# Kernel optimization log

Hardware: AMD Instinct MI355X
Metric: run time of the kernel (lower is better)

## Reference

```python
import jax, jax.numpy as jnp
import numpy as np

B, T, D, H, W = 256, 512, 64, 128, 256

def _init_linear(key, out_dim, in_dim):
    lim = 1.0 / np.sqrt(in_dim)
    return jax.random.uniform(key, (out_dim, in_dim), jnp.float32, -lim, lim)

def setup_inputs():
    key = jax.random.key(0)
    ks = jax.random.split(key, 12)
    inp = {}
    inp['ts'] = jnp.arange(T, dtype=jnp.float32)
    for n, k in zip(['coeffs_d', 'coeffs_c', 'coeffs_b', 'coeffs_a'], ks[:4]):
        inp[n] = jax.random.normal(k, (B, T - 1, D), jnp.float32) * 0.05
    # initial MLP: D -> W -> W -> H (relu hidden, identity final)
    inp['i_w0'] = _init_linear(ks[4], W, D); inp['i_b0'] = jnp.zeros((W,), jnp.float32)
    inp['i_w1'] = _init_linear(ks[5], W, W); inp['i_b1'] = jnp.zeros((W,), jnp.float32)
    inp['i_w2'] = _init_linear(ks[6], H, W); inp['i_b2'] = jnp.zeros((H,), jnp.float32)
    # func MLP: H -> W -> W -> H*D (softplus hidden, tanh final)
    inp['f_w0'] = _init_linear(ks[7], W, H); inp['f_b0'] = jnp.zeros((W,), jnp.float32)
    inp['f_w1'] = _init_linear(ks[8], W, W); inp['f_b1'] = jnp.zeros((W,), jnp.float32)
    inp['f_w2'] = _init_linear(ks[9], H * D, W); inp['f_b2'] = jnp.zeros((H * D,), jnp.float32)
    # readout linear: H -> 1
    inp['l_w'] = _init_linear(ks[10], 1, H); inp['l_b'] = jnp.zeros((1,), jnp.float32)
    return inp

def reference(ts, coeffs_d, coeffs_c, coeffs_b, coeffs_a,
              i_w0, i_b0, i_w1, i_b1, i_w2, i_b2,
              f_w0, f_b0, f_w1, f_b1, f_w2, f_b2,
              l_w, l_b):
    dt = ts[1] - ts[0]
    # cubic spline value at t=ts[0]: interval 0, frac 0 -> a[0]
    x0 = coeffs_a[:, 0, :]  # [B, D]
    h = jax.nn.relu(x0 @ i_w0.T + i_b0)
    h = jax.nn.relu(h @ i_w1.T + i_b1)
    y0 = h @ i_w2.T + i_b2  # [B, H]

    def step(carry, _):
        t, y = carry
        # cubic spline derivative at t: b + 2c*frac + 3d*frac^2 on interval idx
        idx = jnp.clip(jnp.searchsorted(ts, t, side='right') - 1, 0, T - 2)
        frac = t - ts[idx]
        deriv = coeffs_b[:, idx] + 2.0 * coeffs_c[:, idx] * frac + 3.0 * coeffs_d[:, idx] * (frac * frac)  # [B, D]
        # vector field f(y): [B, H, D]
        g = jax.nn.softplus(y @ f_w0.T + f_b0)
        g = jax.nn.softplus(g @ f_w1.T + f_b1)
        f = jnp.tanh(g @ f_w2.T + f_b2).reshape(B, H, D)
        # Euler step: y1 = y + (f @ dX/dt) * dt
        y1 = y + jnp.einsum('bhd,bd->bh', f, deriv) * dt
        return (t + dt, y1), y1

    _, ys = jax.lax.scan(step, (ts[0], y0), None, length=T)
    # prediction = sigmoid(linear(ys[-1]))[0], per batch element
    return jax.nn.sigmoid(ys[-1] @ l_w.T + l_b)[:, 0]  # [B]
```

## Files before the change

### kernel.cpp

```cpp
#include <hip/hip_runtime.h>
#include <hip/hip_bf16.h>
#include <stdint.h>


#define BB 256
#define DD 64
#define HH 128
#define WW 256
#define HD 8192
#define TSTEPS 512
#define PAD_Y 152
#define PAD_G 280
#define PAD_DV 68

typedef __bf16 bf16x8 __attribute__((ext_vector_type(8)));
typedef __bf16 bf16x4 __attribute__((ext_vector_type(4)));
typedef float f32x4 __attribute__((ext_vector_type(4)));

__device__ __forceinline__ float softplus_f(float x) {
  return (x > 15.f) ? x : __logf(1.f + __expf(x));
}
__device__ __forceinline__ float tanh_f(float x) {
  float e = __expf(2.f * x);
  return 1.f - 2.f / (e + 1.f);
}
__device__ __forceinline__ float aloadf(const float* p) {
  return __hip_atomic_load(p, __ATOMIC_RELAXED, __HIP_MEMORY_SCOPE_AGENT);
}
__device__ __forceinline__ void astoref(float* p, float v) {
  __hip_atomic_store(p, v, __ATOMIC_RELAXED, __HIP_MEMORY_SCOPE_AGENT);
}
__device__ __forceinline__ uint32_t aloadu(const uint32_t* p) {
  return __hip_atomic_load(p, __ATOMIC_RELAXED, __HIP_MEMORY_SCOPE_AGENT);
}
__device__ __forceinline__ void astoreu(uint32_t* p, uint32_t v) {
  __hip_atomic_store(p, v, __ATOMIC_RELAXED, __HIP_MEMORY_SCOPE_AGENT);
}

__global__ void prep_kernel(const float* __restrict__ w0, const float* __restrict__ w1,
                            const float* __restrict__ w2,
                            __bf16* __restrict__ w0b, __bf16* __restrict__ w1b,
                            __bf16* __restrict__ w2b) {
  int stride = gridDim.x * blockDim.x;
  int i0 = blockIdx.x * blockDim.x + threadIdx.x;
  for (int i = i0; i < WW * HH; i += stride) w0b[i] = (__bf16)w0[i];
  for (int i = i0; i < WW * WW; i += stride) w1b[i] = (__bf16)w1[i];
  for (int i = i0; i < HD * WW; i += stride) w2b[i] = (__bf16)w2[i];
}

__global__ __launch_bounds__(256) void init_kernel(
    const float* __restrict__ ca, const float* __restrict__ iw0, const float* __restrict__ ib0,
    const float* __restrict__ iw1, const float* __restrict__ ib1,
    const float* __restrict__ iw2, const float* __restrict__ ib2,
    float* __restrict__ y0) {
  __shared__ float x0[DD];
  __shared__ float h0[WW];
  __shared__ float h1[WW];
  int b = blockIdx.x, t = threadIdx.x;
  if (t < DD) x0[t] = ca[((size_t)b * 511) * DD + t];
  __syncthreads();
  float a = ib0[t];
  for (int d = 0; d < DD; ++d) a = fmaf(x0[d], iw0[t * DD + d], a);
  h0[t] = fmaxf(a, 0.f);
  __syncthreads();
  a = ib1[t];
  for (int d = 0; d < WW; ++d) a = fmaf(h0[d], iw1[t * WW + d], a);
  h1[t] = fmaxf(a, 0.f);
  __syncthreads();
  if (t < HH) {
    a = ib2[t];
    for (int d = 0; d < WW; ++d) a = fmaf(h1[d], iw2[t * WW + d], a);
    y0[b * HH + t] = a;
  }
}

__global__ __launch_bounds__(512, 2) void step_persist(
    const __bf16* __restrict__ w0b, const __bf16* __restrict__ w1b, const __bf16* __restrict__ w2b,
    const float* __restrict__ fb0, const float* __restrict__ fb1, const float* __restrict__ fb2,
    const float* __restrict__ cbp, const float* __restrict__ ccp, const float* __restrict__ cdp,
    float* __restrict__ yA, float* __restrict__ pk, uint32_t* __restrict__ yflag)
{
  __shared__ __align__(16) __bf16 yb[32 * PAD_Y];
  __shared__ __align__(16) __bf16 g0s[32 * PAD_G];
  __shared__ __align__(16) __bf16 g1s[32 * PAD_G];
  __shared__ __align__(16) float dv[32 * PAD_DV];
  __shared__ float pbuf[8 * 32];

  const int tid = threadIdx.x;
  const int wv = tid >> 6;
  const int l = tid & 63;
  const int l16 = l & 15;
  const int lq = l >> 4;

  const int wid = blockIdx.x;
  const int grp = wid >> 5;
  const int j = wid & 31;
  const int rb = grp * 32;
  const int c0 = j * 256;

  bf16x8 w0f[4][2], w1f[8][2], w2f[8][2];
  #pragma unroll
  for (int c = 0; c < 2; ++c) {
    int col = wv * 32 + c * 16 + l16;
    #pragma unroll
    for (int kb = 0; kb < 4; ++kb)
      w0f[kb][c] = *(const bf16x8*)&w0b[col * HH + kb * 32 + lq * 8];
    #pragma unroll
    for (int kb = 0; kb < 8; ++kb)
      w1f[kb][c] = *(const bf16x8*)&w1b[col * WW + kb * 32 + lq * 8];
    #pragma unroll
    for (int kb = 0; kb < 8; ++kb)
      w2f[kb][c] = *(const bf16x8*)&w2b[(size_t)(c0 + col) * WW + kb * 32 + lq * 8];
  }
  f32x4 b0r[2], b1r[2], b2r[2];
  #pragma unroll
  for (int c = 0; c < 2; ++c) {
    b0r[c] = *(const f32x4*)&fb0[wv * 32 + c * 16 + lq * 4];
    b1r[c] = *(const f32x4*)&fb1[wv * 32 + c * 16 + lq * 4];
    b2r[c] = *(const f32x4*)&fb2[c0 + wv * 32 + c * 16 + lq * 4];
  }

  float yreg = 0.f;
  int myidx = 0;
  if (tid < 128) {
    int r = tid & 31, hl = tid >> 5;
    myidx = (rb + r) * HH + (4 * j + hl);
    yreg = yA[myidx];
    astoref(&pk[myidx], yreg);
  }
  __syncthreads();
  if (tid == 0) astoreu(&yflag[grp * 32 + j], 1u);

  const int ps = tid & 31;
  const int pw = tid >> 5;
  const uint32_t* myflag = &yflag[grp * 32 + ps];

  for (int k = 0; k < TSTEPS; ++k) {
    const uint32_t want = (uint32_t)(k + 1);
    const float* src = pk + (size_t)(k & 1) * (BB * HH);
    float* dst = pk + (size_t)((k + 1) & 1) * (BB * HH);

    float dreg[4];
    {
      int kk = (k <= 510) ? k : 510;
      #pragma unroll
      for (int q = 0; q < 4; ++q) {
        int i = tid + q * 512;
        int r = i >> 6, d = i & (DD - 1);
        int off = ((rb + r) * 511 + kk) * DD + d;
        float v = cbp[off];
        if (k == 511) v += 2.f * ccp[off] + 3.f * cdp[off];
        dreg[q] = v;
      }
    }

    {
      int spins = 0;
      while (aloadu(myflag) < want) {
        __builtin_amdgcn_s_sleep(1);
        if (++spins > (1 << 20)) break;
      }
      __asm__ __volatile__("" ::: "memory");
      #pragma unroll
      for (int r2 = 0; r2 < 2; ++r2) {
        int row = 2 * pw + r2;
        const float* ysrc = &src[(rb + row) * HH + 4 * ps];
        bf16x4 o;
        #pragma unroll
        for (int q = 0; q < 4; ++q) o[q] = (__bf16)aloadf(&ysrc[q]);
        *(bf16x4*)&yb[row * PAD_Y + 4 * ps] = o;
      }
    }
    __syncthreads();

    {
      f32x4 acc[2][2] = {};
      #pragma unroll
      for (int kb = 0; kb < 4; ++kb) {
        bf16x8 y0 = *(const bf16x8*)&yb[l16 * PAD_Y + kb * 32 + lq * 8];
        bf16x8 y1 = *(const bf16x8*)&yb[(16 + l16) * PAD_Y + kb * 32 + lq * 8];
        #pragma unroll
        for (int c = 0; c < 2; ++c) {
          acc[c][0] = __builtin_amdgcn_mfma_f32_16x16x32_bf16(w0f[kb][c], y0, acc[c][0], 0, 0, 0);
          acc[c][1] = __builtin_amdgcn_mfma_f32_16x16x32_bf16(w0f[kb][c], y1, acc[c][1], 0, 0, 0);
        }
      }
      #pragma unroll
      for (int c = 0; c < 2; ++c)
        #pragma unroll
        for (int bt = 0; bt < 2; ++bt) {
          bf16x4 o;
          #pragma unroll
          for (int r = 0; r < 4; ++r)
            o[r] = (__bf16)softplus_f(acc[c][bt][r] + b0r[c][r]);
          *(bf16x4*)&g0s[(bt * 16 + l16) * PAD_G + wv * 32 + c * 16 + lq * 4] = o;
        }
    }
    #pragma unroll
    for (int q = 0; q < 4; ++q) {
      int i = tid + q * 512;
      dv[(i >> 6) * PAD_DV + (i & (DD - 1))] = dreg[q];
    }
    __syncthreads();

    {
      f32x4 acc[2][2] = {};
      #pragma unroll
      for (int kb = 0; kb < 8; ++kb) {
        bf16x8 a0 = *(const bf16x8*)&g0s[l16 * PAD_G + kb * 32 + lq * 8];
        bf16x8 a1 = *(const bf16x8*)&g0s[(16 + l16) * PAD_G + kb * 32 + lq * 8];
        #pragma unroll
        for (int c = 0; c < 2; ++c) {
          acc[c][0] = __builtin_amdgcn_mfma_f32_16x16x32_bf16(w1f[kb][c], a0, acc[c][0], 0, 0, 0);
          acc[c][1] = __builtin_amdgcn_mfma_f32_16x16x32_bf16(w1f[kb][c], a1, acc[c][1], 0, 0, 0);
        }
      }
      #pragma unroll
      for (int c = 0; c < 2; ++c)
        #pragma unroll
        for (int bt = 0; bt < 2; ++bt) {
          bf16x4 o;
          #pragma unroll
          for (int r = 0; r < 4; ++r)
            o[r] = (__bf16)softplus_f(acc[c][bt][r] + b1r[c][r]);
          *(bf16x4*)&g1s[(bt * 16 + l16) * PAD_G + wv * 32 + c * 16 + lq * 4] = o;
        }
    }
    __syncthreads();

    {
      f32x4 acc[2][2] = {};
      #pragma unroll
      for (int kb = 0; kb < 8; ++kb) {
        bf16x8 a0 = *(const bf16x8*)&g1s[l16 * PAD_G + kb * 32 + lq * 8];
        bf16x8 a1 = *(const bf16x8*)&g1s[(16 + l16) * PAD_G + kb * 32 + lq * 8];
        #pragma unroll
        for (int c = 0; c < 2; ++c) {
          acc[c][0] = __builtin_amdgcn_mfma_f32_16x16x32_bf16(w2f[kb][c], a0, acc[c][0], 0, 0, 0);
          acc[c][1] = __builtin_amdgcn_mfma_f32_16x16x32_bf16(w2f[kb][c], a1, acc[c][1], 0, 0, 0);
        }
      }
      #pragma unroll
      for (int bt = 0; bt < 2; ++bt) {
        float p = 0.f;
        #pragma unroll
        for (int c = 0; c < 2; ++c) {
          f32x4 dvv = *(const f32x4*)&dv[(bt * 16 + l16) * PAD_DV +
                                         (wv & 1) * 32 + c * 16 + lq * 4];
          #pragma unroll
          for (int r = 0; r < 4; ++r) {
            float f = tanh_f(acc[c][bt][r] + b2r[c][r]);
            p = fmaf(f, dvv[r], p);
          }
        }
        p += __shfl_xor(p, 16);
        p += __shfl_xor(p, 32);
        if (l < 16) pbuf[wv * 32 + bt * 16 + l] = p;
      }
    }
    __syncthreads();

    if (tid < 128) {
      int hl = tid >> 5, r = tid & 31;
      yreg += pbuf[(2 * hl) * 32 + r] + pbuf[(2 * hl + 1) * 32 + r];
      astoref(&dst[myidx], yreg);
    }
    __syncthreads();
    if (tid == 0) astoreu(&yflag[grp * 32 + j], (uint32_t)(k + 2));
  }

  if (tid < 128) yA[myidx] = yreg;
}

__global__ __launch_bounds__(256) void final_kernel(const float* __restrict__ y,
                                                    const float* __restrict__ lw,
                                                    const float* __restrict__ lb,
                                                    float* __restrict__ out) {
  int b = threadIdx.x;
  float a = lb[0];
  for (int h = 0; h < HH; ++h) a = fmaf(y[b * HH + h], lw[h], a);
  out[b] = 1.f / (1.f + __expf(-a));
}

extern "C" void kernel_launch(void* const* d_in, const int* in_sizes, int n_in,
                              void* d_out, int out_size, void* d_ws, size_t ws_size,
                              hipStream_t stream) {
  const float* cdp = (const float*)d_in[1];
  const float* ccp = (const float*)d_in[2];
  const float* cbp = (const float*)d_in[3];
  const float* cap = (const float*)d_in[4];
  const float* iw0 = (const float*)d_in[5];
  const float* ib0 = (const float*)d_in[6];
  const float* iw1 = (const float*)d_in[7];
  const float* ib1 = (const float*)d_in[8];
  const float* iw2 = (const float*)d_in[9];
  const float* ib2 = (const float*)d_in[10];
  const float* fw0 = (const float*)d_in[11];
  const float* fb0 = (const float*)d_in[12];
  const float* fw1 = (const float*)d_in[13];
  const float* fb1 = (const float*)d_in[14];
  const float* fw2 = (const float*)d_in[15];
  const float* fb2 = (const float*)d_in[16];
  const float* lw  = (const float*)d_in[17];
  const float* lb  = (const float*)d_in[18];

  char* ws = (char*)d_ws;
  __bf16* w0b = (__bf16*)(ws);
  __bf16* w1b = (__bf16*)(ws + 65536);
  __bf16* w2b = (__bf16*)(ws + 196608);
  float* yA = (float*)(ws + 4390912);
  float* pk = (float*)(ws + 4521984);
  uint32_t* yflag = (uint32_t*)(ws + 4784128);

  hipMemsetAsync(yflag, 0, 1024, stream);
  prep_kernel<<<512, 256, 0, stream>>>(fw0, fw1, fw2, w0b, w1b, w2b);
  init_kernel<<<BB, 256, 0, stream>>>(cap, iw0, ib0, iw1, ib1, iw2, ib2, yA);
  step_persist<<<256, 512, 0, stream>>>(w0b, w1b, w2b, fb0, fb1, fb2,
                                        cbp, ccp, cdp, yA, pk, yflag);
  final_kernel<<<1, 256, 0, stream>>>(yA, lw, lb, (float*)d_out);

  (void)in_sizes; (void)n_in; (void)out_size; (void)ws_size;
}
```

Baseline: 3.682 ms.

## Move half of W2 fragments to LDS and load spline derivatives directly into registers

Half of the per-wave W2 weight fragments move from VGPRs into a 64KB LDS buffer that is read once per k-block, which lowers register pressure. The spline derivative is no longer staged through a shared dv array. Each lane now loads the f32x4 values it needs straight from global memory, which removes one __syncthreads per step. Biases are folded into the MFMA accumulator initialisation. The cost is extra LDS reads on every step and a larger LDS footprint, which may limit the two-blocks-per-CU launch bound.

```diff
diff --git a/kernel.cpp b/kernel.cpp
--- a/kernel.cpp
+++ b/kernel.cpp
@@ -11,7 +11,6 @@
 #define TSTEPS 512
 #define PAD_Y 152
 #define PAD_G 280
-#define PAD_DV 68
 
 typedef __bf16 bf16x8 __attribute__((ext_vector_type(8)));
 typedef __bf16 bf16x4 __attribute__((ext_vector_type(4)));
@@ -80,10 +79,10 @@
     const float* __restrict__ cbp, const float* __restrict__ ccp, const float* __restrict__ cdp,
     float* __restrict__ yA, float* __restrict__ pk, uint32_t* __restrict__ yflag)
 {
+  __shared__ __align__(16) __bf16 w2l[32768];
   __shared__ __align__(16) __bf16 yb[32 * PAD_Y];
   __shared__ __align__(16) __bf16 g0s[32 * PAD_G];
   __shared__ __align__(16) __bf16 g1s[32 * PAD_G];
-  __shared__ __align__(16) float dv[32 * PAD_DV];
   __shared__ float pbuf[8 * 32];
 
   const int tid = threadIdx.x;
@@ -98,7 +97,18 @@
   const int rb = grp * 32;
   const int c0 = j * 256;
 
-  bf16x8 w0f[4][2], w1f[8][2], w2f[8][2];
+  for (int it = 0; it < 8; ++it) {
+    int blk = tid + it * 512;
+    int kq = blk >> 7, cl = blk & 127;
+    int wv2 = cl >> 4, l16b = cl & 15;
+    int kb = kq >> 2, lq2 = kq & 3;
+    int col = c0 + wv2 * 32 + l16b;
+    *(bf16x8*)&w2l[blk * 8] =
+        *(const bf16x8*)&w2b[(size_t)col * WW + kb * 32 + lq2 * 8];
+  }
+  const int w2base = lq * 1024 + wv * 128 + l16 * 8;
+
+  bf16x8 w0f[4][2], w1f[8][2], w2f1[8];
   #pragma unroll
   for (int c = 0; c < 2; ++c) {
     int col = wv * 32 + c * 16 + l16;
@@ -108,9 +118,12 @@
     #pragma unroll
     for (int kb = 0; kb < 8; ++kb)
       w1f[kb][c] = *(const bf16x8*)&w1b[col * WW + kb * 32 + lq * 8];
+  }
+  {
+    int col = c0 + wv * 32 + 16 + l16;
     #pragma unroll
     for (int kb = 0; kb < 8; ++kb)
-      w2f[kb][c] = *(const bf16x8*)&w2b[(size_t)(c0 + col) * WW + kb * 32 + lq * 8];
+      w2f1[kb] = *(const bf16x8*)&w2b[(size_t)col * WW + kb * 32 + lq * 8];
   }
   f32x4 b0r[2], b1r[2], b2r[2];
   #pragma unroll
@@ -119,6 +132,11 @@
     b1r[c] = *(const f32x4*)&fb1[wv * 32 + c * 16 + lq * 4];
     b2r[c] = *(const f32x4*)&fb2[c0 + wv * 32 + c * 16 + lq * 4];
   }
+
+  size_t cb2[2];
+  #pragma unroll
+  for (int bt = 0; bt < 2; ++bt)
+    cb2[bt] = ((size_t)(rb + bt * 16 + l16) * 511) * DD + (wv & 1) * 32 + lq * 4;
 
   float yreg = 0.f;
   int myidx = 0;
@@ -140,18 +158,23 @@
     const float* src = pk + (size_t)(k & 1) * (BB * HH);
     float* dst = pk + (size_t)((k + 1) & 1) * (BB * HH);
 
-    float dreg[4];
-    {
-      int kk = (k <= 510) ? k : 510;
-      #pragma unroll
-      for (int q = 0; q < 4; ++q) {
-        int i = tid + q * 512;
-        int r = i >> 6, d = i & (DD - 1);
-        int off = ((rb + r) * 511 + kk) * DD + d;
-        float v = cbp[off];
-        if (k == 511) v += 2.f * ccp[off] + 3.f * cdp[off];
-        dreg[q] = v;
-      }
+    f32x4 dvv[2][2];
+    {
+      size_t ko = (size_t)((k <= 510) ? k : 510) * DD;
+      #pragma unroll
+      for (int bt = 0; bt < 2; ++bt)
+        #pragma unroll
+        for (int c = 0; c < 2; ++c) {
+          size_t off = cb2[bt] + ko + c * 16;
+          dvv[bt][c] = *(const f32x4*)&cbp[off];
+          if (k == 511) {
+            f32x4 cc = *(const f32x4*)&ccp[off];
+            f32x4 dd = *(const f32x4*)&cdp[off];
+            #pragma unroll
+            for (int r = 0; r < 4; ++r)
+              dvv[bt][c][r] += 2.f * cc[r] + 3.f * dd[r];
+          }
+        }
     }
 
     {
@@ -174,7 +197,9 @@
     __syncthreads();
 
     {
-      f32x4 acc[2][2] = {};
+      f32x4 acc[2][2];
+      #pragma unroll
+      for (int c = 0; c < 2; ++c) { acc[c][0] = b0r[c]; acc[c][1] = b0r[c]; }
       #pragma unroll
       for (int kb = 0; kb < 4; ++kb) {
         bf16x8 y0 = *(const bf16x8*)&yb[l16 * PAD_Y + kb * 32 + lq * 8];
@@ -192,19 +217,16 @@
           bf16x4 o;
           #pragma unroll
           for (int r = 0; r < 4; ++r)
-            o[r] = (__bf16)softplus_f(acc[c][bt][r] + b0r[c][r]);
+            o[r] = (__bf16)softplus_f(acc[c][bt][r]);
           *(bf16x4*)&g0s[(bt * 16 + l16) * PAD_G + wv * 32 + c * 16 + lq * 4] = o;
         }
     }
-    #pragma unroll
-    for (int q = 0; q < 4; ++q) {
-      int i = tid + q * 512;
-      dv[(i >> 6) * PAD_DV + (i & (DD - 1))] = dreg[q];
-    }
-    __syncthreads();
-
-    {
-      f32x4 acc[2][2] = {};
+    __syncthreads();
+
+    {
+      f32x4 acc[2][2];
+      #pragma unroll
+      for (int c = 0; c < 2; ++c) { acc[c][0] = b1r[c]; acc[c][1] = b1r[c]; }
       #pragma unroll
       for (int kb = 0; kb < 8; ++kb) {
         bf16x8 a0 = *(const bf16x8*)&g0s[l16 * PAD_G + kb * 32 + lq * 8];
@@ -222,35 +244,35 @@
           bf16x4 o;
           #pragma unroll
           for (int r = 0; r < 4; ++r)
-            o[r] = (__bf16)softplus_f(acc[c][bt][r] + b1r[c][r]);
+            o[r] = (__bf16)softplus_f(acc[c][bt][r]);
           *(bf16x4*)&g1s[(bt * 16 + l16) * PAD_G + wv * 32 + c * 16 + lq * 4] = o;
         }
     }
     __syncthreads();
 
     {
-      f32x4 acc[2][2] = {};
+      f32x4 acc[2][2];
+      #pragma unroll
+      for (int c = 0; c < 2; ++c) { acc[c][0] = b2r[c]; acc[c][1] = b2r[c]; }
       #pragma unroll
       for (int kb = 0; kb < 8; ++kb) {
         bf16x8 a0 = *(const bf16x8*)&g1s[l16 * PAD_G + kb * 32 + lq * 8];
         bf16x8 a1 = *(const bf16x8*)&g1s[(16 + l16) * PAD_G + kb * 32 + lq * 8];
-        #pragma unroll
-        for (int c = 0; c < 2; ++c) {
-          acc[c][0] = __builtin_amdgcn_mfma_f32_16x16x32_bf16(w2f[kb][c], a0, acc[c][0], 0, 0, 0);
-          acc[c][1] = __builtin_amdgcn_mfma_f32_16x16x32_bf16(w2f[kb][c], a1, acc[c][1], 0, 0, 0);
-        }
+        bf16x8 wf0 = *(const bf16x8*)&w2l[w2base + kb * 4096];
+        acc[0][0] = __builtin_amdgcn_mfma_f32_16x16x32_bf16(wf0, a0, acc[0][0], 0, 0, 0);
+        acc[0][1] = __builtin_amdgcn_mfma_f32_16x16x32_bf16(wf0, a1, acc[0][1], 0, 0, 0);
+        acc[1][0] = __builtin_amdgcn_mfma_f32_16x16x32_bf16(w2f1[kb], a0, acc[1][0], 0, 0, 0);
+        acc[1][1] = __builtin_amdgcn_mfma_f32_16x16x32_bf16(w2f1[kb], a1, acc[1][1], 0, 0, 0);
       }
       #pragma unroll
       for (int bt = 0; bt < 2; ++bt) {
         float p = 0.f;
         #pragma unroll
         for (int c = 0; c < 2; ++c) {
-          f32x4 dvv = *(const f32x4*)&dv[(bt * 16 + l16) * PAD_DV +
-                                         (wv & 1) * 32 + c * 16 + lq * 4];
           #pragma unroll
           for (int r = 0; r < 4; ++r) {
-            float f = tanh_f(acc[c][bt][r] + b2r[c][r]);
-            p = fmaf(f, dvv[r], p);
+            float f = tanh_f(acc[c][bt][r]);
+            p = fmaf(f, dvv[bt][c][r], p);
           }
         }
         p += __shfl_xor(p, 16);
```

After: 3.681 ms. Within noise of the previous version (-0.0%).
